# Kernel optimization log

Measured on AMD Instinct MI355X. Metric: run time of the kernel, lower is better.

Reference implementation:

```python
import jax, jax.numpy as jnp
import numpy as np
import math

B, T, E, H, QL, SUB = 4, 2048, 64, 8, 6, 64  # batch, win_len, n_embd, n_head, q_len, sub_len


def _row_mask(index, sub_len, win_len):
    log_l = math.ceil(np.log2(sub_len))
    mask = np.zeros(win_len, dtype=np.float32)
    if (win_len // sub_len) * 2 * log_l > index:
        mask[: index + 1] = 1
    else:
        while index >= 0:
            if index - log_l + 1 < 0:
                mask[:index] = 1
                break
            mask[index - log_l + 1 : index + 1] = 1
            for i in range(log_l):
                new_index = index - log_l + 1 - 2 ** i
                if index - new_index <= sub_len and new_index >= 0:
                    mask[new_index] = 1
            index -= sub_len
    return mask


def _log_mask(win_len, sub_len):
    m = np.zeros((win_len, win_len), dtype=np.float32)
    for i in range(win_len):
        m[i] = _row_mask(i, sub_len, win_len)
    return m.reshape(1, 1, win_len, win_len)


def setup_inputs() -> dict:
    key = jax.random.key(0)
    ks = jax.random.split(key, 4)
    x = jax.random.normal(ks[0], (B, T, E), dtype=jnp.float32)
    Wqk = jax.random.normal(ks[1], (2 * H * E, E, QL), dtype=jnp.float32) * 0.02
    bqk = jnp.zeros((2 * H * E,), dtype=jnp.float32)
    Wv = jax.random.normal(ks[2], (E, H * E), dtype=jnp.float32) * 0.02
    bv = jnp.zeros((H * E,), dtype=jnp.float32)
    Wp = jax.random.normal(ks[3], (H * E, E), dtype=jnp.float32) * 0.02
    bp = jnp.zeros((E,), dtype=jnp.float32)
    mask = jnp.asarray(_log_mask(T, SUB).astype(bool))  # [1,1,T,T] bool
    return {"x": x, "Wqk": Wqk, "bqk": bqk, "Wv": Wv, "bv": bv,
            "Wp": Wp, "bp": bp, "mask": mask}


def reference(x, Wqk, bqk, Wv, bv, Wp, bp, mask):
    b, t, e = x.shape
    h = Wv.shape[1] // e
    ql = Wqk.shape[-1]

    # value projection (Conv1D rf=1 == dense)
    value = x @ Wv + bv                              # [B,T,H*E]

    # causal conv1d QK projection: left-pad by q_len-1
    xc = jnp.transpose(x, (0, 2, 1))                 # [B,E,T]
    qk = jax.lax.conv_general_dilated(
        xc, Wqk, window_strides=(1,), padding=[(ql - 1, 0)],
        dimension_numbers=("NCH", "OIH", "NCH"))    # [B,2*H*E,T]
    qk = qk + bqk[None, :, None]
    qk = jnp.transpose(qk, (0, 2, 1))                # [B,T,2*H*E]
    query, key_ = jnp.split(qk, 2, axis=2)

    q = query.reshape(b, t, h, e).transpose(0, 2, 1, 3)   # [B,H,T,E]
    k = key_.reshape(b, t, h, e).transpose(0, 2, 3, 1)    # [B,H,E,T]
    v = value.reshape(b, t, h, e).transpose(0, 2, 1, 3)   # [B,H,T,E]

    pre = jnp.einsum("bhqe,bhek->bhqk", q, k) / jnp.sqrt(jnp.asarray(e, x.dtype))
    m = mask[:, :, :t, :t].astype(pre.dtype)
    pre = pre * m + (-1e9) * (1.0 - m)
    attn_weights = jax.nn.softmax(pre, axis=-1)           # [B,H,T,T]
    # dropout p=0.0 -> identity
    attn = jnp.einsum("bhqk,bhke->bhqe", attn_weights, v)  # [B,H,T,E]
    attn = attn.transpose(0, 2, 1, 3).reshape(b, t, h * e)
    out = attn @ Wp + bp                                  # [B,T,E]
    return out, attn_weights
```

## Files before the change

### kernel.cpp

```cpp
#include <hip/hip_runtime.h>
#include <hip/hip_bf16.h>


typedef __attribute__((ext_vector_type(8))) short bf16x8;
typedef __attribute__((ext_vector_type(4))) float f32x4;

#define MFMA16(a, b, c) __builtin_amdgcn_mfma_f32_16x16x32_bf16((a), (b), (c), 0, 0, 0)

static __device__ __forceinline__ bool sparse_pred(int r, int c) {
  int d = r - c;
  if (d < 0) return false;
  int o = d & 63;
  int j = c + o;
  bool inS = (o <= 7) || (o == 9) || (o == 13) || (o == 21) || (o == 37);
  return (j >= 5) ? inS : (o >= 1);
}

struct KF {
  bf16x8 a[8];
};

static __device__ __forceinline__ KF loadK(const __hip_bfloat16* __restrict__ kbh, int ct, int lm,
                                           int lq) {
  KF f;
  const __hip_bfloat16* kbase = kbh + (size_t)ct * 64 * 64;
#pragma unroll
  for (int nb = 0; nb < 4; ++nb) {
    const __hip_bfloat16* krow = kbase + (size_t)(16 * nb + lm) * 64;
    f.a[2 * nb] = *reinterpret_cast<const bf16x8*>(krow + lq * 8);
    f.a[2 * nb + 1] = *reinterpret_cast<const bf16x8*>(krow + 32 + lq * 8);
  }
  return f;
}

__global__ void prep_kernel(const float* __restrict__ Wqk, const float* __restrict__ Wv,
                            __hip_bfloat16* __restrict__ Wt_qk, __hip_bfloat16* __restrict__ Wv_t) {
  int idx = blockIdx.x * 256 + threadIdx.x;
  if (idx < 1024 * 384) {
    int o = idx / 384, kidx = idx - o * 384;
    int kk = kidx >> 6, i = kidx & 63;
    Wt_qk[idx] = __float2bfloat16(Wqk[(o * 64 + i) * 6 + kk]);
  } else {
    int j = idx - 1024 * 384;
    int n = j >> 6, k = j & 63;
    Wv_t[j] = __float2bfloat16(Wv[k * 512 + n]);
  }
}

__global__ __launch_bounds__(256, 4) void proj_kernel(
    const float* __restrict__ x, const float* __restrict__ bqk, const float* __restrict__ bv,
    const __hip_bfloat16* __restrict__ Wt_qk, const __hip_bfloat16* __restrict__ Wv_t,
    __hip_bfloat16* __restrict__ q_bf, __hip_bfloat16* __restrict__ k_bf,
    __hip_bfloat16* __restrict__ v_bf) {
  const int tokTile = blockIdx.x;
  const int chTile = blockIdx.y;
  const int gt0 = tokTile * 64;
  const int b = gt0 >> 11;
  const int t0 = gt0 & 2047;
  const int thr = threadIdx.x;
  __shared__ __align__(16) __hip_bfloat16 xwin[69][72];
  __shared__ __align__(16) __hip_bfloat16 vt[64][72];

  for (int u = thr; u < 69 * 64; u += 256) {
    int row = u >> 6, i = u & 63;
    int t = t0 - 5 + row;
    float v = (t >= 0) ? x[((size_t)b * 2048 + t) * 64 + i] : 0.f;
    xwin[row][i] = __float2bfloat16(v);
  }
  __syncthreads();

  const int wave = thr >> 6, lane = thr & 63;
  const int lm = lane & 15, lq = lane >> 4;
  f32x4 acc[4];
#pragma unroll
  for (int nb = 0; nb < 4; ++nb) acc[nb] = (f32x4){0.f, 0.f, 0.f, 0.f};

  if (chTile < 16) {
    const int ch0 = chTile * 64;
    for (int kc = 0; kc < 12; ++kc) {
      int k0 = kc * 32 + lq * 8;
      int kk = k0 >> 6, i0 = k0 & 63;
      bf16x8 a = *reinterpret_cast<const bf16x8*>(&xwin[16 * wave + lm + kk][i0]);
#pragma unroll
      for (int nb = 0; nb < 4; ++nb) {
        bf16x8 bb =
            *reinterpret_cast<const bf16x8*>(&Wt_qk[(size_t)(ch0 + 16 * nb + lm) * 384 + k0]);
        acc[nb] = MFMA16(a, bb, acc[nb]);
      }
    }
#pragma unroll
    for (int nb = 0; nb < 4; ++nb) {
      int e = 16 * nb + lm;
      float bias = bqk[chTile * 64 + e];
#pragma unroll
      for (int reg = 0; reg < 4; ++reg)
        vt[16 * wave + lq * 4 + reg][e] = __float2bfloat16(acc[nb][reg] + bias);
    }
    __syncthreads();
    const int half = (chTile >> 3) & 1;
    const int h = chTile & 7;
    __hip_bfloat16* dst = half ? k_bf : q_bf;
    for (int u = thr; u < 512; u += 256) {
      int row = u >> 3, c8 = u & 7;
      *reinterpret_cast<uint4*>(dst + ((size_t)((b * 8 + h) * 2048 + t0 + row)) * 64 + c8 * 8) =
          *reinterpret_cast<const uint4*>(&vt[row][c8 * 8]);
    }
  } else {
    const int nv0 = (chTile - 16) * 64;
    for (int kc = 0; kc < 2; ++kc) {
      int i0 = kc * 32 + lq * 8;
      bf16x8 a = *reinterpret_cast<const bf16x8*>(&xwin[16 * wave + lm + 5][i0]);
#pragma unroll
      for (int nb = 0; nb < 4; ++nb) {
        bf16x8 bb = *reinterpret_cast<const bf16x8*>(&Wv_t[(size_t)(nv0 + 16 * nb + lm) * 64 + i0]);
        acc[nb] = MFMA16(a, bb, acc[nb]);
      }
    }
#pragma unroll
    for (int nb = 0; nb < 4; ++nb) {
      int e = 16 * nb + lm;
      float bias = bv[nv0 + e];
#pragma unroll
      for (int reg = 0; reg < 4; ++reg)
        vt[e][16 * wave + lq * 4 + reg] = __float2bfloat16(acc[nb][reg] + bias);
    }
    __syncthreads();
    const int h = chTile - 16;
    for (int u = thr; u < 512; u += 256) {
      int e = u >> 3, c8 = u & 7;
      *reinterpret_cast<uint4*>(v_bf + ((size_t)((b * 8 + h) * 64 + e)) * 2048 + t0 + c8 * 8) =
          *reinterpret_cast<const uint4*>(&vt[e][c8 * 8]);
    }
  }
}

__global__ __launch_bounds__(64, 4) void attn_kernel(
    const __hip_bfloat16* __restrict__ q_bf, const __hip_bfloat16* __restrict__ k_bf,
    const __hip_bfloat16* __restrict__ v_bf,
    float* __restrict__ attn, float* __restrict__ attnout) {
  const int bh = blockIdx.y;
  const int bz = blockIdx.z;
  const int lane = threadIdx.x;
  const int lm = lane & 15, lq = lane >> 4;

  __shared__ __align__(16) __hip_bfloat16 psw[16 * 72];

  const int b2 = bh >> 3, h = bh & 7;
  const __hip_bfloat16* kbh = k_bf + (size_t)bh * 2048 * 64;
  const __hip_bfloat16* vbh = v_bf + (size_t)bh * 64 * 2048;

  unsigned pm[4];
  {
    const int S[12] = {0, 1, 2, 3, 4, 5, 6, 7, 9, 13, 21, 37};
#pragma unroll
    for (int reg = 0; reg < 4; ++reg) {
      int r64 = 16 * bz + 4 * lq + reg;
      unsigned long long m = 0;
#pragma unroll
      for (int i = 0; i < 12; ++i) m |= 1ull << ((r64 - S[i]) & 63);
      unsigned p = 0;
#pragma unroll
      for (int nb = 0; nb < 4; ++nb) p |= (unsigned)((m >> (16 * nb + lm)) & 1ull) << nb;
      pm[reg] = p;
    }
  }

  for (int task = 0; task < 2; ++task) {
    const int rt = (task == 0) ? (int)blockIdx.x : 31 - (int)blockIdx.x;
    const int r0 = rt * 64;
    const bool causal = (rt < 6);

    const __hip_bfloat16* qrow = q_bf + ((size_t)bh * 2048 + r0 + 16 * bz + lm) * 64;
    bf16x8 qa0 = *reinterpret_cast<const bf16x8*>(qrow + lq * 8);
    bf16x8 qa1 = *reinterpret_cast<const bf16x8*>(qrow + 32 + lq * 8);

    float lsum[4] = {0.f, 0.f, 0.f, 0.f};
    {
      KF kc = loadK(kbh, 0, lm, lq);
      for (int ct = 0; ct <= rt; ++ct) {
        KF kn = kc;
        if (ct < rt) kn = loadK(kbh, ct + 1, lm, lq);
        f32x4 cf[4];
#pragma unroll
        for (int nb = 0; nb < 4; ++nb) {
          f32x4 c = (f32x4){0.f, 0.f, 0.f, 0.f};
          c = MFMA16(qa0, kc.a[2 * nb], c);
          c = MFMA16(qa1, kc.a[2 * nb + 1], c);
          cf[nb] = c;
        }
        const bool diag = (ct == rt);
        if (causal && !diag) {
#pragma unroll
          for (int nb = 0; nb < 4; ++nb)
#pragma unroll
            for (int reg = 0; reg < 4; ++reg) lsum[reg] += __expf(cf[nb][reg] * 0.125f);
        } else if (causal) {
#pragma unroll
          for (int nb = 0; nb < 4; ++nb) {
            const int col = ct * 64 + 16 * nb + lm;
#pragma unroll
            for (int reg = 0; reg < 4; ++reg) {
              const int row = r0 + 16 * bz + 4 * lq + reg;
              lsum[reg] += (col <= row) ? __expf(cf[nb][reg] * 0.125f) : 0.f;
            }
          }
        } else if (ct == 0) {
#pragma unroll
          for (int nb = 0; nb < 4; ++nb) {
            const int col = 16 * nb + lm;
#pragma unroll
            for (int reg = 0; reg < 4; ++reg) {
              const int row = r0 + 16 * bz + 4 * lq + reg;
              lsum[reg] += sparse_pred(row, col) ? __expf(cf[nb][reg] * 0.125f) : 0.f;
            }
          }
        } else if (!diag) {
#pragma unroll
          for (int nb = 0; nb < 4; ++nb)
#pragma unroll
            for (int reg = 0; reg < 4; ++reg)
              lsum[reg] += ((pm[reg] >> nb) & 1u) ? __expf(cf[nb][reg] * 0.125f) : 0.f;
        } else {
#pragma unroll
          for (int nb = 0; nb < 4; ++nb) {
            const int col = ct * 64 + 16 * nb + lm;
#pragma unroll
            for (int reg = 0; reg < 4; ++reg) {
              const int row = r0 + 16 * bz + 4 * lq + reg;
              bool p = ((pm[reg] >> nb) & 1u) && (col <= row);
              lsum[reg] += p ? __expf(cf[nb][reg] * 0.125f) : 0.f;
            }
          }
        }
        kc = kn;
      }
    }
    float inv[4];
#pragma unroll
    for (int reg = 0; reg < 4; ++reg) {
      float v = lsum[reg];
      v += __shfl_xor(v, 1);
      v += __shfl_xor(v, 2);
      v += __shfl_xor(v, 4);
      v += __shfl_xor(v, 8);
      inv[reg] = 1.f / v;
    }

    f32x4 oacc[4];
#pragma unroll
    for (int eb = 0; eb < 4; ++eb) oacc[eb] = (f32x4){0.f, 0.f, 0.f, 0.f};
    float* arow0 = attn + ((size_t)bh * 2048 + r0 + 16 * bz + 4 * lq) * 2048;

    KF kc = loadK(kbh, 0, lm, lq);
    for (int ct = 0; ct <= rt; ++ct) {
      KF kn = kc;
      if (ct < rt) kn = loadK(kbh, ct + 1, lm, lq);
      f32x4 cf[4];
#pragma unroll
      for (int nb = 0; nb < 4; ++nb) {
        f32x4 c = (f32x4){0.f, 0.f, 0.f, 0.f};
        c = MFMA16(qa0, kc.a[2 * nb], c);
        c = MFMA16(qa1, kc.a[2 * nb + 1], c);
        cf[nb] = c;
      }
      const bool diag = (ct == rt);
#pragma unroll
      for (int nb = 0; nb < 4; ++nb) {
        const int col = ct * 64 + 16 * nb + lm;
#pragma unroll
        for (int reg = 0; reg < 4; ++reg) {
          const int row = r0 + 16 * bz + 4 * lq + reg;
          bool p;
          if (causal) {
            p = diag ? (col <= row) : true;
          } else if (ct == 0) {
            p = sparse_pred(row, col);
          } else {
            p = (pm[reg] >> nb) & 1u;
            if (diag) p = p && (col <= row);
          }
          float w = p ? __expf(cf[nb][reg] * 0.125f) * inv[reg] : 0.f;
          psw[(4 * lq + reg) * 72 + 16 * nb + lm] = __float2bfloat16(w);
          arow0[(size_t)reg * 2048 + col] = w;
        }
      }
      bf16x8 pa0 = *reinterpret_cast<const bf16x8*>(psw + lm * 72 + lq * 8);
      bf16x8 pa1 = *reinterpret_cast<const bf16x8*>(psw + lm * 72 + 32 + lq * 8);
      const __hip_bfloat16* vbase = vbh + ct * 64;
#pragma unroll
      for (int eb = 0; eb < 4; ++eb) {
        const __hip_bfloat16* vrow = vbase + (size_t)(16 * eb + lm) * 2048;
        bf16x8 vb0 = *reinterpret_cast<const bf16x8*>(vrow + lq * 8);
        bf16x8 vb1 = *reinterpret_cast<const bf16x8*>(vrow + 32 + lq * 8);
        oacc[eb] = MFMA16(pa0, vb0, oacc[eb]);
        oacc[eb] = MFMA16(pa1, vb1, oacc[eb]);
      }
      kc = kn;
    }

#pragma unroll
    for (int eb = 0; eb < 4; ++eb)
#pragma unroll
      for (int reg = 0; reg < 4; ++reg) {
        int row = r0 + 16 * bz + lq * 4 + reg;
        attnout[((size_t)(b2 * 2048 + row)) * 512 + h * 64 + 16 * eb + lm] = oacc[eb][reg];
      }
  }
}

__global__ __launch_bounds__(256, 4) void outproj_kernel(const float* __restrict__ attnout,
                                                         const float* __restrict__ Wp,
                                                         const float* __restrict__ bp,
                                                         float* __restrict__ out) {
  __shared__ __align__(16) float wp_s[128][64];
  const int thr = threadIdx.x;
  const int wave = thr >> 6, lane = thr & 63;
  const int row0 = blockIdx.x * 16 + wave * 4;
  float acc[4] = {0.f, 0.f, 0.f, 0.f};
  for (int kt = 0; kt < 4; ++kt) {
    __syncthreads();
    for (int u = thr; u < 2048; u += 256) {
      int r = u >> 4, c4 = (u & 15) * 4;
      *reinterpret_cast<float4*>(&wp_s[r][c4]) =
          *reinterpret_cast<const float4*>(&Wp[(size_t)(kt * 128 + r) * 64 + c4]);
    }
    __syncthreads();
    for (int k4 = 0; k4 < 32; ++k4) {
      float wv0 = wp_s[k4 * 4 + 0][lane];
      float wv1 = wp_s[k4 * 4 + 1][lane];
      float wv2 = wp_s[k4 * 4 + 2][lane];
      float wv3 = wp_s[k4 * 4 + 3][lane];
#pragma unroll
      for (int rr = 0; rr < 4; ++rr) {
        const float4 a = *reinterpret_cast<const float4*>(
            &attnout[(size_t)(row0 + rr) * 512 + kt * 128 + k4 * 4]);
        acc[rr] += a.x * wv0 + a.y * wv1 + a.z * wv2 + a.w * wv3;
      }
    }
  }
  const float bias = bp[lane];
#pragma unroll
  for (int rr = 0; rr < 4; ++rr) out[(size_t)(row0 + rr) * 64 + lane] = acc[rr] + bias;
}

extern "C" void kernel_launch(void* const* d_in, const int* in_sizes, int n_in, void* d_out,
                              int out_size, void* d_ws, size_t ws_size, hipStream_t stream) {
  (void)in_sizes;
  (void)n_in;
  (void)out_size;
  (void)ws_size;
  const float* x = (const float*)d_in[0];
  const float* Wqk = (const float*)d_in[1];
  const float* bqk = (const float*)d_in[2];
  const float* Wv = (const float*)d_in[3];
  const float* bv = (const float*)d_in[4];
  const float* Wp = (const float*)d_in[5];
  const float* bp = (const float*)d_in[6];

  float* out = (float*)d_out;
  float* attn = out + (size_t)4 * 2048 * 64;

  char* ws = (char*)d_ws;
  __hip_bfloat16* q_bf = (__hip_bfloat16*)(ws);
  __hip_bfloat16* k_bf = (__hip_bfloat16*)(ws + (size_t)8 * 1024 * 1024);
  __hip_bfloat16* v_bf = (__hip_bfloat16*)(ws + (size_t)16 * 1024 * 1024);
  float* attnout = (float*)(ws + (size_t)24 * 1024 * 1024);
  __hip_bfloat16* Wt_qk = (__hip_bfloat16*)(ws + (size_t)40 * 1024 * 1024);
  __hip_bfloat16* Wv_t = (__hip_bfloat16*)(ws + (size_t)41 * 1024 * 1024);

  hipLaunchKernelGGL(prep_kernel, dim3(1664), dim3(256), 0, stream, Wqk, Wv, Wt_qk, Wv_t);
  hipLaunchKernelGGL(proj_kernel, dim3(128, 24), dim3(256), 0, stream, x, bqk, bv, Wt_qk, Wv_t,
                     q_bf, k_bf, v_bf);
  hipLaunchKernelGGL(attn_kernel, dim3(16, 32, 4), dim3(64), 0, stream, q_bf, k_bf, v_bf, attn,
                     attnout);
  hipLaunchKernelGGL(outproj_kernel, dim3(512), dim3(256), 0, stream, attnout, Wp, bp, out);
}
```

Baseline: 786.5 us.

## Merge four row-slice waves into one block and prefetch V fragments

Replaces the four single-wave blocks (grid z dimension) with one 256-thread block whose four waves each handle a 16-row slice of the same 64-row tile. Each wave gets its own LDS slice for the probability tile. Waves sharing K/V tiles in one workgroup can get better cache locality and there are fewer blocks to schedule. V fragments for the next column tile are now prefetched into registers alongside K, hiding load latency at the cost of more VGPRs under launch bounds (256,2).

After: 765.3 us. -2.7%, faster.

```diff
diff --git a/kernel.cpp b/kernel.cpp
--- a/kernel.cpp
+++ b/kernel.cpp
@@ -29,6 +29,23 @@
     const __hip_bfloat16* krow = kbase + (size_t)(16 * nb + lm) * 64;
     f.a[2 * nb] = *reinterpret_cast<const bf16x8*>(krow + lq * 8);
     f.a[2 * nb + 1] = *reinterpret_cast<const bf16x8*>(krow + 32 + lq * 8);
+  }
+  return f;
+}
+
+struct VF {
+  bf16x8 a[8];
+};
+
+static __device__ __forceinline__ VF loadV(const __hip_bfloat16* __restrict__ vbh, int ct, int lm,
+                                           int lq) {
+  VF f;
+  const __hip_bfloat16* vbase = vbh + ct * 64;
+#pragma unroll
+  for (int eb = 0; eb < 4; ++eb) {
+    const __hip_bfloat16* vrow = vbase + (size_t)(16 * eb + lm) * 2048;
+    f.a[2 * eb] = *reinterpret_cast<const bf16x8*>(vrow + lq * 8);
+    f.a[2 * eb + 1] = *reinterpret_cast<const bf16x8*>(vrow + 32 + lq * 8);
   }
   return f;
 }
@@ -134,16 +151,17 @@
   }
 }
 
-__global__ __launch_bounds__(64, 4) void attn_kernel(
+__global__ __launch_bounds__(256, 2) void attn_kernel(
     const __hip_bfloat16* __restrict__ q_bf, const __hip_bfloat16* __restrict__ k_bf,
     const __hip_bfloat16* __restrict__ v_bf,
     float* __restrict__ attn, float* __restrict__ attnout) {
   const int bh = blockIdx.y;
-  const int bz = blockIdx.z;
-  const int lane = threadIdx.x;
+  const int wave = threadIdx.x >> 6;
+  const int lane = threadIdx.x & 63;
   const int lm = lane & 15, lq = lane >> 4;
 
-  __shared__ __align__(16) __hip_bfloat16 psw[16 * 72];
+  __shared__ __align__(16) __hip_bfloat16 psw[4][16 * 72];
+  __hip_bfloat16* pw = psw[wave];
 
   const int b2 = bh >> 3, h = bh & 7;
   const __hip_bfloat16* kbh = k_bf + (size_t)bh * 2048 * 64;
@@ -154,7 +172,7 @@
     const int S[12] = {0, 1, 2, 3, 4, 5, 6, 7, 9, 13, 21, 37};
 #pragma unroll
     for (int reg = 0; reg < 4; ++reg) {
-      int r64 = 16 * bz + 4 * lq + reg;
+      int r64 = 16 * wave + 4 * lq + reg;
       unsigned long long m = 0;
 #pragma unroll
       for (int i = 0; i < 12; ++i) m |= 1ull << ((r64 - S[i]) & 63);
@@ -170,7 +188,7 @@
     const int r0 = rt * 64;
     const bool causal = (rt < 6);
 
-    const __hip_bfloat16* qrow = q_bf + ((size_t)bh * 2048 + r0 + 16 * bz + lm) * 64;
+    const __hip_bfloat16* qrow = q_bf + ((size_t)bh * 2048 + r0 + 16 * wave + lm) * 64;
     bf16x8 qa0 = *reinterpret_cast<const bf16x8*>(qrow + lq * 8);
     bf16x8 qa1 = *reinterpret_cast<const bf16x8*>(qrow + 32 + lq * 8);
 
@@ -200,7 +218,7 @@
             const int col = ct * 64 + 16 * nb + lm;
 #pragma unroll
             for (int reg = 0; reg < 4; ++reg) {
-              const int row = r0 + 16 * bz + 4 * lq + reg;
+              const int row = r0 + 16 * wave + 4 * lq + reg;
               lsum[reg] += (col <= row) ? __expf(cf[nb][reg] * 0.125f) : 0.f;
             }
           }
@@ -210,7 +228,7 @@
             const int col = 16 * nb + lm;
 #pragma unroll
             for (int reg = 0; reg < 4; ++reg) {
-              const int row = r0 + 16 * bz + 4 * lq + reg;
+              const int row = r0 + 16 * wave + 4 * lq + reg;
               lsum[reg] += sparse_pred(row, col) ? __expf(cf[nb][reg] * 0.125f) : 0.f;
             }
           }
@@ -226,7 +244,7 @@
             const int col = ct * 64 + 16 * nb + lm;
 #pragma unroll
             for (int reg = 0; reg < 4; ++reg) {
-              const int row = r0 + 16 * bz + 4 * lq + reg;
+              const int row = r0 + 16 * wave + 4 * lq + reg;
               bool p = ((pm[reg] >> nb) & 1u) && (col <= row);
               lsum[reg] += p ? __expf(cf[nb][reg] * 0.125f) : 0.f;
             }
@@ -249,12 +267,17 @@
     f32x4 oacc[4];
 #pragma unroll
     for (int eb = 0; eb < 4; ++eb) oacc[eb] = (f32x4){0.f, 0.f, 0.f, 0.f};
-    float* arow0 = attn + ((size_t)bh * 2048 + r0 + 16 * bz + 4 * lq) * 2048;
+    float* arow0 = attn + ((size_t)bh * 2048 + r0 + 16 * wave + 4 * lq) * 2048;
 
     KF kc = loadK(kbh, 0, lm, lq);
+    VF vc = loadV(vbh, 0, lm, lq);
     for (int ct = 0; ct <= rt; ++ct) {
       KF kn = kc;
-      if (ct < rt) kn = loadK(kbh, ct + 1, lm, lq);
+      VF vn = vc;
+      if (ct < rt) {
+        kn = loadK(kbh, ct + 1, lm, lq);
+        vn = loadV(vbh, ct + 1, lm, lq);
+      }
       f32x4 cf[4];
 #pragma unroll
       for (int nb = 0; nb < 4; ++nb) {
@@ -269,7 +292,7 @@
         const int col = ct * 64 + 16 * nb + lm;
 #pragma unroll
         for (int reg = 0; reg < 4; ++reg) {
-          const int row = r0 + 16 * bz + 4 * lq + reg;
+          const int row = r0 + 16 * wave + 4 * lq + reg;
           bool p;
           if (causal) {
             p = diag ? (col <= row) : true;
@@ -280,29 +303,26 @@
             if (diag) p = p && (col <= row);
           }
           float w = p ? __expf(cf[nb][reg] * 0.125f) * inv[reg] : 0.f;
-          psw[(4 * lq + reg) * 72 + 16 * nb + lm] = __float2bfloat16(w);
+          pw[(4 * lq + reg) * 72 + 16 * nb + lm] = __float2bfloat16(w);
           arow0[(size_t)reg * 2048 + col] = w;
         }
       }
-      bf16x8 pa0 = *reinterpret_cast<const bf16x8*>(psw + lm * 72 + lq * 8);
-      bf16x8 pa1 = *reinterpret_cast<const bf16x8*>(psw + lm * 72 + 32 + lq * 8);
-      const __hip_bfloat16* vbase = vbh + ct * 64;
+      bf16x8 pa0 = *reinterpret_cast<const bf16x8*>(pw + lm * 72 + lq * 8);
+      bf16x8 pa1 = *reinterpret_cast<const bf16x8*>(pw + lm * 72 + 32 + lq * 8);
 #pragma unroll
       for (int eb = 0; eb < 4; ++eb) {
-        const __hip_bfloat16* vrow = vbase + (size_t)(16 * eb + lm) * 2048;
-        bf16x8 vb0 = *reinterpret_cast<const bf16x8*>(vrow + lq * 8);
-        bf16x8 vb1 = *reinterpret_cast<const bf16x8*>(vrow + 32 + lq * 8);
-        oacc[eb] = MFMA16(pa0, vb0, oacc[eb]);
-        oacc[eb] = MFMA16(pa1, vb1, oacc[eb]);
+        oacc[eb] = MFMA16(pa0, vc.a[2 * eb], oacc[eb]);
+        oacc[eb] = MFMA16(pa1, vc.a[2 * eb + 1], oacc[eb]);
       }
       kc = kn;
+      vc = vn;
     }
 
 #pragma unroll
     for (int eb = 0; eb < 4; ++eb)
 #pragma unroll
       for (int reg = 0; reg < 4; ++reg) {
-        int row = r0 + 16 * bz + lq * 4 + reg;
+        int row = r0 + 16 * wave + lq * 4 + reg;
         attnout[((size_t)(b2 * 2048 + row)) * 512 + h * 64 + 16 * eb + lm] = oacc[eb][reg];
       }
   }
@@ -371,7 +391,7 @@
   hipLaunchKernelGGL(prep_kernel, dim3(1664), dim3(256), 0, stream, Wqk, Wv, Wt_qk, Wv_t);
   hipLaunchKernelGGL(proj_kernel, dim3(128, 24), dim3(256), 0, stream, x, bqk, bv, Wt_qk, Wv_t,
                      q_bf, k_bf, v_bf);
-  hipLaunchKernelGGL(attn_kernel, dim3(16, 32, 4), dim3(64), 0, stream, q_bf, k_bf, v_bf, attn,
+  hipLaunchKernelGGL(attn_kernel, dim3(16, 32), dim3(256), 0, stream, q_bf, k_bf, v_bf, attn,
                      attnout);
   hipLaunchKernelGGL(outproj_kernel, dim3(512), dim3(256), 0, stream, attnout, Wp, bp, out);
 }
```
